# Kernel tuning notes

Measured on AMD Instinct MI355X. Metric: run time of the kernel, lower is better.

## Reference

```python
import jax, jax.numpy as jnp
import numpy as np

DILATION = 1  # module init dilation


def _pd_indexing1d(x, d, dilation):
    # x: (B, C, T) float; d: (B, 1, T) float pitch-dependent dilation factors
    B, C, T = x.shape
    dil = jnp.clip((d * dilation).astype(jnp.int32), 1)          # (B,1,T), min 1
    idx = jnp.arange(T, dtype=jnp.int32)[None, None, :]          # (1,1,T)
    idxP = jnp.abs(idx - dil) % T                                # past indices
    idxF0 = idx + dil
    # torch sets overflowed idx to -(idx % T) - 1, i.e. wraps to T - 1 - (idx % T)
    idxF = jnp.where(idxF0 >= T, T - 1 - (idxF0 % T), idxF0)     # future indices
    xP = jnp.take_along_axis(x, jnp.broadcast_to(idxP, x.shape), axis=2)
    xF = jnp.take_along_axis(x, jnp.broadcast_to(idxF, x.shape), axis=2)
    return xP, x, xF


def setup_inputs() -> dict:
    key = jax.random.key(0)
    k1, k2, k3, k4, k5, k6 = jax.random.split(key, 6)
    B, Cin, Cout, T = 8, 512, 512, 8192
    x = jax.random.normal(k1, (B, Cin, T), dtype=jnp.float32)
    d = jax.random.uniform(k2, (B, 1, T), dtype=jnp.float32)
    s = 1.0 / np.sqrt(Cin)
    W0 = jax.random.uniform(k3, (Cout, Cin), jnp.float32, -s, s)  # conv with bias
    b0 = jax.random.uniform(k4, (Cout,), jnp.float32, -s, s)
    W1 = jax.random.uniform(k5, (Cout, Cin), jnp.float32, -s, s)  # no bias
    W2 = jax.random.uniform(k6, (Cout, Cin), jnp.float32, -s, s)  # no bias
    return {"x": x, "d": d, "W0": W0, "b0": b0, "W1": W1, "W2": W2}


def reference(x, d, W0, b0, W1, W2):
    xP, xC, xF = _pd_indexing1d(x, d, DILATION)
    # three 1x1 convs (channel-mixing matmuls), summed; bias only on first conv
    out = jnp.einsum('oc,bct->bot', W0, xP) + b0[None, :, None]
    out = out + jnp.einsum('oc,bct->bot', W1, xC)
    out = out + jnp.einsum('oc,bct->bot', W2, xF)
    return out
```

## Files before the change

kernel.cpp:

```cpp
#include <hip/hip_runtime.h>

#define TT 8192
#define CIN 512
#define COUT 512
#define NB 8
#define KTOT 1536
#define NT 24

typedef __attribute__((ext_vector_type(4))) float f32x4;
typedef __attribute__((ext_vector_type(8))) short bf16x8;
typedef __attribute__((ext_vector_type(8))) unsigned short u16x8;

#define GLD16(g, l) __builtin_amdgcn_global_load_lds(                      \
    (const __attribute__((address_space(1))) void*)(g),                    \
    (__attribute__((address_space(3))) void*)(l), 16, 0, 0)

#define CFENCE() asm volatile("" ::: "memory")
#define SBAR() do { CFENCE(); __builtin_amdgcn_s_barrier(); CFENCE(); } while (0)
#define VMCNT4() asm volatile("s_waitcnt vmcnt(4)" ::: "memory")
#define VMCNT0() asm volatile("s_waitcnt vmcnt(0)" ::: "memory")
#define MFMA(a_, b_, c_) __builtin_amdgcn_mfma_f32_16x16x32_bf16((a_), (b_), (c_), 0, 0, 0)

__device__ inline unsigned short f2bf(float f) {
  union { float f; unsigned int u; } v; v.f = f;
  unsigned int u = v.u;
  unsigned int r = (u + 0x7FFFu + ((u >> 16) & 1u)) >> 16;
  return (unsigned short)r;
}

__global__ void k_convert_w(const float* __restrict__ W0, const float* __restrict__ W1,
                            const float* __restrict__ W2, unsigned short* __restrict__ Wb) {
  int i = blockIdx.x * 256 + threadIdx.x;
  if (i >= COUT * CIN) return;
  const float* Ws = blockIdx.y == 0 ? W0 : (blockIdx.y == 1 ? W1 : W2);
  int o = i >> 9, c = i & 511;
  Wb[(size_t)o * KTOT + blockIdx.y * CIN + c] = f2bf(Ws[i]);
}

__global__ void k_transpose(const float* __restrict__ x, unsigned short* __restrict__ xbT,
                            int b_base) {
  int b = b_base + blockIdx.z;
  const float* xb = x + (size_t)b * CIN * TT;
  unsigned short* xo = xbT + (size_t)blockIdx.z * TT * CIN;
  __shared__ float tile[64][65];
  int t0 = blockIdx.x * 64, c0 = blockIdx.y * 64;
  int tid = threadIdx.x;
#pragma unroll
  for (int it = 0; it < 16; ++it) {
    int L = it * 256 + tid;
    int c = L >> 6, t = L & 63;
    tile[c][t] = xb[(size_t)(c0 + c) * TT + (t0 + t)];
  }
  __syncthreads();
#pragma unroll
  for (int it = 0; it < 16; ++it) {
    int L = it * 256 + tid;
    int t = L >> 6, c = L & 63;
    xo[(size_t)(t0 + t) * CIN + (c0 + c)] = f2bf(tile[c][t]);
  }
}

__global__ __launch_bounds__(512) void k_gemm256(
    const unsigned short* __restrict__ Wb, const unsigned short* __restrict__ xbT,
    const float* __restrict__ d, const float* __restrict__ bias,
    float* __restrict__ out) {
  __shared__ __align__(16) unsigned short As[2][256 * 64];
  __shared__ __align__(16) unsigned short Bs[2][256 * 64];
  const int b = blockIdx.x;
  const int t0 = (blockIdx.y >> 1) * 256;
  const int row0 = (blockIdx.y & 1) * 256;
  const unsigned short* xb = xbT + (size_t)b * TT * CIN;
  const int tid = threadIdx.x;
  const int lane = tid & 63, wid = tid >> 6;
  const int wr = wid >> 2, wc = wid & 3;
  const int l15 = lane & 15, kg = lane >> 4;

  const int srow = tid >> 3;
  const int cSrc8 = (((tid & 7) ^ ((tid >> 4) & 7))) * 8;
  int aOff[4];
  int bOff[3][4];
#pragma unroll
  for (int j = 0; j < 4; ++j) {
    int r = j * 64 + srow;
    aOff[j] = (row0 + r) * KTOT + cSrc8;
    int t = t0 + r;
    float dv = d[(size_t)b * TT + t];
    int dil = (int)dv; if (dil < 1) dil = 1;
    int p = t - dil; if (p < 0) p = -p; p &= (TT - 1);
    int f0 = t + dil;
    int f = (f0 >= TT) ? (TT - 1 - (f0 & (TT - 1))) : f0;
    bOff[0][j] = p * CIN + cSrc8;
    bOff[1][j] = t * CIN + cSrc8;
    bOff[2][j] = f * CIN + cSrc8;
  }

  const int s7 = l15 >> 1;
  const int chunk0 = (kg ^ (s7 & 3)) + (s7 & 4);
  const int dK = (l15 & 8) ? -32 : 32;
  int aRd[2][4], bRd[2][2];
#pragma unroll
  for (int mh = 0; mh < 2; ++mh)
#pragma unroll
    for (int mi = 0; mi < 4; ++mi)
      aRd[mh][mi] = (wr * 128 + mh * 64 + mi * 16 + l15) * 64 + chunk0 * 8;
#pragma unroll
  for (int nh = 0; nh < 2; ++nh)
#pragma unroll
    for (int ni = 0; ni < 2; ++ni)
      bRd[nh][ni] = (wc * 64 + nh * 32 + ni * 16 + l15) * 64 + chunk0 * 8;

#define STAGE_A2(tc_, buf_, jp_) do {                                         \
    _Pragma("unroll") for (int j = 2 * (jp_); j < 2 * (jp_) + 2; ++j)         \
      GLD16(Wb + aOff[j] + (tc_) * 64, &As[buf_][j * 4096 + wid * 512]);      \
  } while (0)
#define STAGE_B2(tc_, buf_, jp_) do {                                         \
    _Pragma("unroll") for (int j = 2 * (jp_); j < 2 * (jp_) + 2; ++j)         \
      GLD16(xb + bOff[(tc_) >> 3][j] + ((tc_) & 7) * 64,                      \
            &Bs[buf_][j * 4096 + wid * 512]);                                 \
  } while (0)

  STAGE_A2(0, 0, 0); STAGE_A2(0, 0, 1);
  STAGE_B2(0, 0, 0); STAGE_B2(0, 0, 1);
  STAGE_B2(1, 1, 0); STAGE_B2(1, 1, 1);
  VMCNT4();
  SBAR();

  bf16x8 af0[4][2], af1[4][2], bfr[2][2];
  f32x4 acc[8][4] = {};

#pragma unroll 2
  for (int tc = 0; tc < NT; ++tc) {
    const int cur = tc & 1;
#pragma unroll
    for (int mi = 0; mi < 4; ++mi) {
      af0[mi][0] = *(const bf16x8*)&As[cur][aRd[0][mi]];
      af0[mi][1] = *(const bf16x8*)&As[cur][aRd[0][mi] + dK];
    }
#pragma unroll
    for (int ni = 0; ni < 2; ++ni) {
      bfr[ni][0] = *(const bf16x8*)&Bs[cur][bRd[0][ni]];
      bfr[ni][1] = *(const bf16x8*)&Bs[cur][bRd[0][ni] + dK];
    }
    if (tc + 1 < NT) STAGE_A2(tc + 1, cur ^ 1, 0);
    SBAR();
    __builtin_amdgcn_s_setprio(1);
#pragma unroll
    for (int mi = 0; mi < 4; ++mi)
#pragma unroll
      for (int ni = 0; ni < 2; ++ni) {
        acc[mi][ni] = MFMA(af0[mi][0], bfr[ni][0], acc[mi][ni]);
        acc[mi][ni] = MFMA(af0[mi][1], bfr[ni][1], acc[mi][ni]);
      }
    __builtin_amdgcn_s_setprio(0);
    SBAR();
#pragma unroll
    for (int mi = 0; mi < 4; ++mi) {
      af1[mi][0] = *(const bf16x8*)&As[cur][aRd[1][mi]];
      af1[mi][1] = *(const bf16x8*)&As[cur][aRd[1][mi] + dK];
    }
    if (tc + 1 < NT) STAGE_A2(tc + 1, cur ^ 1, 1);
    SBAR();
    __builtin_amdgcn_s_setprio(1);
#pragma unroll
    for (int mi = 0; mi < 4; ++mi)
#pragma unroll
      for (int ni = 0; ni < 2; ++ni) {
        acc[4 + mi][ni] = MFMA(af1[mi][0], bfr[ni][0], acc[4 + mi][ni]);
        acc[4 + mi][ni] = MFMA(af1[mi][1], bfr[ni][1], acc[4 + mi][ni]);
      }
    __builtin_amdgcn_s_setprio(0);
#pragma unroll
    for (int ni = 0; ni < 2; ++ni) {
      bfr[ni][0] = *(const bf16x8*)&Bs[cur][bRd[1][ni]];
      bfr[ni][1] = *(const bf16x8*)&Bs[cur][bRd[1][ni] + dK];
    }
    SBAR();
    __builtin_amdgcn_s_setprio(1);
#pragma unroll
    for (int mi = 0; mi < 4; ++mi)
#pragma unroll
      for (int ni = 0; ni < 2; ++ni) {
        acc[mi][2 + ni] = MFMA(af0[mi][0], bfr[ni][0], acc[mi][2 + ni]);
        acc[mi][2 + ni] = MFMA(af0[mi][1], bfr[ni][1], acc[mi][2 + ni]);
      }
    __builtin_amdgcn_s_setprio(0);
    if (tc + 2 < NT) { STAGE_B2(tc + 2, cur, 0); STAGE_B2(tc + 2, cur, 1); }
    __builtin_amdgcn_s_setprio(1);
#pragma unroll
    for (int mi = 0; mi < 4; ++mi)
#pragma unroll
      for (int ni = 0; ni < 2; ++ni) {
        acc[4 + mi][2 + ni] = MFMA(af1[mi][0], bfr[ni][0], acc[4 + mi][2 + ni]);
        acc[4 + mi][2 + ni] = MFMA(af1[mi][1], bfr[ni][1], acc[4 + mi][2 + ni]);
      }
    __builtin_amdgcn_s_setprio(0);
    if (tc + 2 < NT) { VMCNT4(); }
    else if (tc + 1 < NT) { VMCNT0(); }
    SBAR();
  }

  float* ob = out + (size_t)b * COUT * TT;
#pragma unroll
  for (int mh = 0; mh < 2; ++mh)
#pragma unroll
    for (int mi = 0; mi < 4; ++mi) {
      int m0 = row0 + wr * 128 + mh * 64 + mi * 16 + kg * 4;
#pragma unroll
      for (int nh = 0; nh < 2; ++nh)
#pragma unroll
        for (int ni = 0; ni < 2; ++ni) {
          int t = t0 + wc * 64 + nh * 32 + ni * 16 + l15;
          f32x4 v = acc[mh * 4 + mi][nh * 2 + ni];
#pragma unroll
          for (int j = 0; j < 4; ++j)
            ob[(size_t)(m0 + j) * TT + t] = v[j] + bias[m0 + j];
        }
    }
}

__global__ __launch_bounds__(256) void k_gemm(
    const unsigned short* __restrict__ Wb, const unsigned short* __restrict__ xbT,
    const float* __restrict__ d, const float* __restrict__ bias,
    float* __restrict__ out, int b_base) {
  __shared__ __align__(16) unsigned short As[128 * 32];
  __shared__ __align__(16) unsigned short Bs[128 * 32];
  int b = b_base + blockIdx.z;
  const unsigned short* xb = xbT + (size_t)blockIdx.z * TT * CIN;
  int row0 = blockIdx.x * 128;
  int t0 = blockIdx.y * 128;
  int tid = threadIdx.x;
  int lane = tid & 63, wid = tid >> 6;
  int wr = wid >> 1, wc = wid & 1;
  int l15 = lane & 15, kg = lane >> 4;
  int rs = tid >> 2, cch = tid & 3;

  const unsigned short* aw[2];
  const unsigned short* bw[2][3];
#pragma unroll
  for (int h = 0; h < 2; ++h) {
    int r = rs + h * 64;
    int cs = cch ^ ((r >> 1) & 3);
    aw[h] = Wb + (size_t)(row0 + r) * KTOT + cs * 8;
    int t = t0 + r;
    float dv = d[(size_t)b * TT + t];
    int dil = (int)dv; if (dil < 1) dil = 1;
    int p = t - dil; if (p < 0) p = -p; p &= (TT - 1);
    int f0 = t + dil;
    int f = (f0 >= TT) ? (TT - 1 - (f0 & (TT - 1))) : f0;
    bw[h][0] = xb + (size_t)p * CIN + cs * 8;
    bw[h][1] = xb + (size_t)t * CIN + cs * 8;
    bw[h][2] = xb + (size_t)f * CIN + cs * 8;
  }
  unsigned short* aDst[2];
  unsigned short* bDst[2];
#pragma unroll
  for (int h = 0; h < 2; ++h) {
    aDst[h] = As + h * 2048 + wid * 512;
    bDst[h] = Bs + h * 2048 + wid * 512;
  }
  int aoff[4], boff[4];
#pragma unroll
  for (int mi = 0; mi < 4; ++mi) {
    int r = wr * 64 + mi * 16 + l15;
    aoff[mi] = r * 32 + (kg ^ ((r >> 1) & 3)) * 8;
  }
#pragma unroll
  for (int ni = 0; ni < 4; ++ni) {
    int r = wc * 64 + ni * 16 + l15;
    boff[ni] = r * 32 + (kg ^ ((r >> 1) & 3)) * 8;
  }
  f32x4 acc[4][4] = {};
#pragma unroll
  for (int s = 0; s < 3; ++s) {
    for (int kt = 0; kt < 16; ++kt) {
      int koff = kt * 32;
#pragma unroll
      for (int h = 0; h < 2; ++h) {
        GLD16(aw[h] + s * CIN + koff, aDst[h]);
        GLD16(bw[h][s] + koff, bDst[h]);
      }
      __syncthreads();
      bf16x8 af[4], bf[4];
#pragma unroll
      for (int mi = 0; mi < 4; ++mi) af[mi] = *(const bf16x8*)(&As[aoff[mi]]);
#pragma unroll
      for (int ni = 0; ni < 4; ++ni) bf[ni] = *(const bf16x8*)(&Bs[boff[ni]]);
#pragma unroll
      for (int mi = 0; mi < 4; ++mi)
#pragma unroll
        for (int ni = 0; ni < 4; ++ni)
          acc[mi][ni] = MFMA(af[mi], bf[ni], acc[mi][ni]);
      __syncthreads();
    }
  }
  float* ob = out + (size_t)b * COUT * TT;
#pragma unroll
  for (int mi = 0; mi < 4; ++mi) {
    int m0 = row0 + wr * 64 + mi * 16 + kg * 4;
#pragma unroll
    for (int ni = 0; ni < 4; ++ni) {
      int t = t0 + wc * 64 + ni * 16 + l15;
#pragma unroll
      for (int j = 0; j < 4; ++j) {
        ob[(size_t)(m0 + j) * TT + t] = acc[mi][ni][j] + bias[m0 + j];
      }
    }
  }
}

extern "C" void kernel_launch(void* const* d_in, const int* in_sizes, int n_in,
                              void* d_out, int out_size, void* d_ws, size_t ws_size,
                              hipStream_t stream) {
  const float* x  = (const float*)d_in[0];
  const float* d  = (const float*)d_in[1];
  const float* W0 = (const float*)d_in[2];
  const float* b0 = (const float*)d_in[3];
  const float* W1 = (const float*)d_in[4];
  const float* W2 = (const float*)d_in[5];
  float* out = (float*)d_out;

  char* ws = (char*)d_ws;
  unsigned short* Wb  = (unsigned short*)ws;
  unsigned short* xbT = (unsigned short*)(ws + (2u << 20));
  const size_t SZ_XBT1 = (size_t)TT * CIN * 2;
  const size_t NEED_FULL = (size_t)(2u << 20) + (size_t)NB * SZ_XBT1;
  const size_t NEED_MIN  = (size_t)(2u << 20) + SZ_XBT1;

  if (ws_size >= NEED_MIN) {
    k_convert_w<<<dim3(1024, 3), 256, 0, stream>>>(W0, W1, W2, Wb);
    if (ws_size >= NEED_FULL) {
      k_transpose<<<dim3(TT / 64, CIN / 64, NB), 256, 0, stream>>>(x, xbT, 0);
      k_gemm256<<<dim3(NB, (TT / 256) * (COUT / 256), 1), 512, 0, stream>>>(
          Wb, xbT, d, b0, out);
    } else {
      for (int b = 0; b < NB; ++b) {
        k_transpose<<<dim3(TT / 64, CIN / 64, 1), 256, 0, stream>>>(x, xbT, b);
        k_gemm<<<dim3(COUT / 128, TT / 128, 1), 256, 0, stream>>>(Wb, xbT, d, b0, out, b);
      }
    }
  } else {
    for (int b = 0; b < NB; ++b) {
      k_transpose<<<dim3(TT / 64, CIN / 64, 1), 256, 0, stream>>>(x, xbT, b);
      k_gemm<<<dim3(COUT / 128, TT / 128, 1), 256, 0, stream>>>(Wb, xbT, d, b0, out, b);
    }
  }
}
```

Baseline: 144.8 us.

## Prefetch A tiles two stages ahead and cut barriers per K-step

Stages the weight (A) tiles two iterations ahead, like B, so both operands share the same double-buffer depth. The first fragment loads for the next iteration move to the end of the current iteration, which removes two of the four barriers in each K-step. An explicit lgkmcnt wait before the remaining barrier guards the LDS reads before that buffer is overwritten. The goal is to cut barrier stalls and overlap global-to-LDS copies with the MFMA work. In exchange more loads are in flight (vmcnt 8), and correctness depends on the hazard ordering of the LDS buffers.

```diff
diff --git a/kernel.cpp b/kernel.cpp
--- a/kernel.cpp
+++ b/kernel.cpp
@@ -17,8 +17,9 @@
 
 #define CFENCE() asm volatile("" ::: "memory")
 #define SBAR() do { CFENCE(); __builtin_amdgcn_s_barrier(); CFENCE(); } while (0)
-#define VMCNT4() asm volatile("s_waitcnt vmcnt(4)" ::: "memory")
+#define VMCNT8() asm volatile("s_waitcnt vmcnt(8)" ::: "memory")
 #define VMCNT0() asm volatile("s_waitcnt vmcnt(0)" ::: "memory")
+#define LGKM0() asm volatile("s_waitcnt lgkmcnt(0)" ::: "memory")
 #define MFMA(a_, b_, c_) __builtin_amdgcn_mfma_f32_16x16x32_bf16((a_), (b_), (c_), 0, 0, 0)
 
 __device__ inline unsigned short f2bf(float f) {
@@ -121,28 +122,33 @@
 
   STAGE_A2(0, 0, 0); STAGE_A2(0, 0, 1);
   STAGE_B2(0, 0, 0); STAGE_B2(0, 0, 1);
+  STAGE_A2(1, 1, 0); STAGE_A2(1, 1, 1);
   STAGE_B2(1, 1, 0); STAGE_B2(1, 1, 1);
-  VMCNT4();
+  VMCNT8();
   SBAR();
 
   bf16x8 af0[4][2], af1[4][2], bfr[2][2];
   f32x4 acc[8][4] = {};
+
+#pragma unroll
+  for (int mi = 0; mi < 4; ++mi) {
+    af0[mi][0] = *(const bf16x8*)&As[0][aRd[0][mi]];
+    af0[mi][1] = *(const bf16x8*)&As[0][aRd[0][mi] + dK];
+  }
+#pragma unroll
+  for (int ni = 0; ni < 2; ++ni) {
+    bfr[ni][0] = *(const bf16x8*)&Bs[0][bRd[0][ni]];
+    bfr[ni][1] = *(const bf16x8*)&Bs[0][bRd[0][ni] + dK];
+  }
 
 #pragma unroll 2
   for (int tc = 0; tc < NT; ++tc) {
     const int cur = tc & 1;
 #pragma unroll
     for (int mi = 0; mi < 4; ++mi) {
-      af0[mi][0] = *(const bf16x8*)&As[cur][aRd[0][mi]];
-      af0[mi][1] = *(const bf16x8*)&As[cur][aRd[0][mi] + dK];
-    }
-#pragma unroll
-    for (int ni = 0; ni < 2; ++ni) {
-      bfr[ni][0] = *(const bf16x8*)&Bs[cur][bRd[0][ni]];
-      bfr[ni][1] = *(const bf16x8*)&Bs[cur][bRd[0][ni] + dK];
-    }
-    if (tc + 1 < NT) STAGE_A2(tc + 1, cur ^ 1, 0);
-    SBAR();
+      af1[mi][0] = *(const bf16x8*)&As[cur][aRd[1][mi]];
+      af1[mi][1] = *(const bf16x8*)&As[cur][aRd[1][mi] + dK];
+    }
     __builtin_amdgcn_s_setprio(1);
 #pragma unroll
     for (int mi = 0; mi < 4; ++mi)
@@ -152,14 +158,6 @@
         acc[mi][ni] = MFMA(af0[mi][1], bfr[ni][1], acc[mi][ni]);
       }
     __builtin_amdgcn_s_setprio(0);
-    SBAR();
-#pragma unroll
-    for (int mi = 0; mi < 4; ++mi) {
-      af1[mi][0] = *(const bf16x8*)&As[cur][aRd[1][mi]];
-      af1[mi][1] = *(const bf16x8*)&As[cur][aRd[1][mi] + dK];
-    }
-    if (tc + 1 < NT) STAGE_A2(tc + 1, cur ^ 1, 1);
-    SBAR();
     __builtin_amdgcn_s_setprio(1);
 #pragma unroll
     for (int mi = 0; mi < 4; ++mi)
@@ -174,7 +172,9 @@
       bfr[ni][0] = *(const bf16x8*)&Bs[cur][bRd[1][ni]];
       bfr[ni][1] = *(const bf16x8*)&Bs[cur][bRd[1][ni] + dK];
     }
+    LGKM0();
     SBAR();
+    if (tc + 2 < NT) { STAGE_A2(tc + 2, cur, 0); STAGE_A2(tc + 2, cur, 1); }
     __builtin_amdgcn_s_setprio(1);
 #pragma unroll
     for (int mi = 0; mi < 4; ++mi)
@@ -194,9 +194,21 @@
         acc[4 + mi][2 + ni] = MFMA(af1[mi][1], bfr[ni][1], acc[4 + mi][2 + ni]);
       }
     __builtin_amdgcn_s_setprio(0);
-    if (tc + 2 < NT) { VMCNT4(); }
+    if (tc + 2 < NT) { VMCNT8(); }
     else if (tc + 1 < NT) { VMCNT0(); }
     SBAR();
+    if (tc + 1 < NT) {
+#pragma unroll
+      for (int mi = 0; mi < 4; ++mi) {
+        af0[mi][0] = *(const bf16x8*)&As[cur ^ 1][aRd[0][mi]];
+        af0[mi][1] = *(const bf16x8*)&As[cur ^ 1][aRd[0][mi] + dK];
+      }
+#pragma unroll
+      for (int ni = 0; ni < 2; ++ni) {
+        bfr[ni][0] = *(const bf16x8*)&Bs[cur ^ 1][bRd[0][ni]];
+        bfr[ni][1] = *(const bf16x8*)&Bs[cur ^ 1][bRd[0][ni] + dK];
+      }
+    }
   }
 
   float* ob = out + (size_t)b * COUT * TT;
```

Result: no change. 145.3 us (+0.3%).

## Load weight fragments directly from global into registers, drop A LDS staging

Applied to the files above, without the earlier changes.

Removes the LDS buffer for the weight (A) tile. Each wave now loads its MFMA A fragments straight from global memory into registers, one K-step ahead, and the vmcnt waits are retuned to the larger number of outstanding loads. This cuts LDS traffic, halves LDS usage and removes two barriers per iteration, which may allow more occupancy. In exchange, weight reads from global are duplicated across the waves sharing rows and now use uncoalesced 16-byte row-strided accesses, and the hand-set vmcnt counts must match the compiler's actual load ordering.

```diff
diff --git a/kernel.cpp b/kernel.cpp
--- a/kernel.cpp
+++ b/kernel.cpp
@@ -17,8 +17,10 @@
 
 #define CFENCE() asm volatile("" ::: "memory")
 #define SBAR() do { CFENCE(); __builtin_amdgcn_s_barrier(); CFENCE(); } while (0)
-#define VMCNT4() asm volatile("s_waitcnt vmcnt(4)" ::: "memory")
+#define VMCNT20() asm volatile("s_waitcnt vmcnt(20)" ::: "memory")
+#define VMCNT16() asm volatile("s_waitcnt vmcnt(16)" ::: "memory")
 #define VMCNT0() asm volatile("s_waitcnt vmcnt(0)" ::: "memory")
+#define LGKM0() asm volatile("s_waitcnt lgkmcnt(0)" ::: "memory")
 #define MFMA(a_, b_, c_) __builtin_amdgcn_mfma_f32_16x16x32_bf16((a_), (b_), (c_), 0, 0, 0)
 
 __device__ inline unsigned short f2bf(float f) {
@@ -64,7 +66,6 @@
     const unsigned short* __restrict__ Wb, const unsigned short* __restrict__ xbT,
     const float* __restrict__ d, const float* __restrict__ bias,
     float* __restrict__ out) {
-  __shared__ __align__(16) unsigned short As[2][256 * 64];
   __shared__ __align__(16) unsigned short Bs[2][256 * 64];
   const int b = blockIdx.x;
   const int t0 = (blockIdx.y >> 1) * 256;
@@ -77,13 +78,10 @@
 
   const int srow = tid >> 3;
   const int cSrc8 = (((tid & 7) ^ ((tid >> 4) & 7))) * 8;
-  int aOff[4];
   int bOff[3][4];
 #pragma unroll
   for (int j = 0; j < 4; ++j) {
-    int r = j * 64 + srow;
-    aOff[j] = (row0 + r) * KTOT + cSrc8;
-    int t = t0 + r;
+    int t = t0 + j * 64 + srow;
     float dv = d[(size_t)b * TT + t];
     int dil = (int)dv; if (dil < 1) dil = 1;
     int p = t - dil; if (p < 0) p = -p; p &= (TT - 1);
@@ -97,76 +95,65 @@
   const int s7 = l15 >> 1;
   const int chunk0 = (kg ^ (s7 & 3)) + (s7 & 4);
   const int dK = (l15 & 8) ? -32 : 32;
-  int aRd[2][4], bRd[2][2];
-#pragma unroll
-  for (int mh = 0; mh < 2; ++mh)
-#pragma unroll
-    for (int mi = 0; mi < 4; ++mi)
-      aRd[mh][mi] = (wr * 128 + mh * 64 + mi * 16 + l15) * 64 + chunk0 * 8;
+  int bRd[2][2];
 #pragma unroll
   for (int nh = 0; nh < 2; ++nh)
 #pragma unroll
     for (int ni = 0; ni < 2; ++ni)
       bRd[nh][ni] = (wc * 64 + nh * 32 + ni * 16 + l15) * 64 + chunk0 * 8;
 
-#define STAGE_A2(tc_, buf_, jp_) do {                                         \
-    _Pragma("unroll") for (int j = 2 * (jp_); j < 2 * (jp_) + 2; ++j)         \
-      GLD16(Wb + aOff[j] + (tc_) * 64, &As[buf_][j * 4096 + wid * 512]);      \
-  } while (0)
+  int aOffA[2][4];
+#pragma unroll
+  for (int mh = 0; mh < 2; ++mh)
+#pragma unroll
+    for (int mi = 0; mi < 4; ++mi)
+      aOffA[mh][mi] = (row0 + wr * 128 + mh * 64 + mi * 16 + l15) * KTOT + kg * 8;
+
 #define STAGE_B2(tc_, buf_, jp_) do {                                         \
     _Pragma("unroll") for (int j = 2 * (jp_); j < 2 * (jp_) + 2; ++j)         \
       GLD16(xb + bOff[(tc_) >> 3][j] + ((tc_) & 7) * 64,                      \
             &Bs[buf_][j * 4096 + wid * 512]);                                 \
   } while (0)
-
-  STAGE_A2(0, 0, 0); STAGE_A2(0, 0, 1);
+#define LOAD_A(mh_, tc_) do {                                                 \
+    _Pragma("unroll") for (int mi = 0; mi < 4; ++mi) {                        \
+      af[mh_][mi][0] = *(const bf16x8*)(Wb + aOffA[mh_][mi] + (tc_) * 64);    \
+      af[mh_][mi][1] = *(const bf16x8*)(Wb + aOffA[mh_][mi] + (tc_) * 64 + 32);\
+    }                                                                         \
+  } while (0)
+
+  bf16x8 af[2][4][2], bfr[2][2];
+  f32x4 acc[8][4] = {};
+
   STAGE_B2(0, 0, 0); STAGE_B2(0, 0, 1);
   STAGE_B2(1, 1, 0); STAGE_B2(1, 1, 1);
-  VMCNT4();
+  LOAD_A(0, 0); LOAD_A(1, 0);
+  VMCNT20();
   SBAR();
-
-  bf16x8 af0[4][2], af1[4][2], bfr[2][2];
-  f32x4 acc[8][4] = {};
 
 #pragma unroll 2
   for (int tc = 0; tc < NT; ++tc) {
     const int cur = tc & 1;
 #pragma unroll
-    for (int mi = 0; mi < 4; ++mi) {
-      af0[mi][0] = *(const bf16x8*)&As[cur][aRd[0][mi]];
-      af0[mi][1] = *(const bf16x8*)&As[cur][aRd[0][mi] + dK];
-    }
-#pragma unroll
     for (int ni = 0; ni < 2; ++ni) {
       bfr[ni][0] = *(const bf16x8*)&Bs[cur][bRd[0][ni]];
       bfr[ni][1] = *(const bf16x8*)&Bs[cur][bRd[0][ni] + dK];
     }
-    if (tc + 1 < NT) STAGE_A2(tc + 1, cur ^ 1, 0);
-    SBAR();
     __builtin_amdgcn_s_setprio(1);
 #pragma unroll
     for (int mi = 0; mi < 4; ++mi)
 #pragma unroll
       for (int ni = 0; ni < 2; ++ni) {
-        acc[mi][ni] = MFMA(af0[mi][0], bfr[ni][0], acc[mi][ni]);
-        acc[mi][ni] = MFMA(af0[mi][1], bfr[ni][1], acc[mi][ni]);
+        acc[mi][ni] = MFMA(af[0][mi][0], bfr[ni][0], acc[mi][ni]);
+        acc[mi][ni] = MFMA(af[0][mi][1], bfr[ni][1], acc[mi][ni]);
       }
     __builtin_amdgcn_s_setprio(0);
-    SBAR();
-#pragma unroll
-    for (int mi = 0; mi < 4; ++mi) {
-      af1[mi][0] = *(const bf16x8*)&As[cur][aRd[1][mi]];
-      af1[mi][1] = *(const bf16x8*)&As[cur][aRd[1][mi] + dK];
-    }
-    if (tc + 1 < NT) STAGE_A2(tc + 1, cur ^ 1, 1);
-    SBAR();
     __builtin_amdgcn_s_setprio(1);
 #pragma unroll
     for (int mi = 0; mi < 4; ++mi)
 #pragma unroll
       for (int ni = 0; ni < 2; ++ni) {
-        acc[4 + mi][ni] = MFMA(af1[mi][0], bfr[ni][0], acc[4 + mi][ni]);
-        acc[4 + mi][ni] = MFMA(af1[mi][1], bfr[ni][1], acc[4 + mi][ni]);
+        acc[4 + mi][ni] = MFMA(af[1][mi][0], bfr[ni][0], acc[4 + mi][ni]);
+        acc[4 + mi][ni] = MFMA(af[1][mi][1], bfr[ni][1], acc[4 + mi][ni]);
       }
     __builtin_amdgcn_s_setprio(0);
 #pragma unroll
@@ -174,28 +161,31 @@
       bfr[ni][0] = *(const bf16x8*)&Bs[cur][bRd[1][ni]];
       bfr[ni][1] = *(const bf16x8*)&Bs[cur][bRd[1][ni] + dK];
     }
+    __builtin_amdgcn_s_setprio(1);
+#pragma unroll
+    for (int mi = 0; mi < 4; ++mi)
+#pragma unroll
+      for (int ni = 0; ni < 2; ++ni) {
+        acc[mi][2 + ni] = MFMA(af[0][mi][0], bfr[ni][0], acc[mi][2 + ni]);
+        acc[mi][2 + ni] = MFMA(af[0][mi][1], bfr[ni][1], acc[mi][2 + ni]);
+      }
+    __builtin_amdgcn_s_setprio(0);
+    if (tc + 1 < NT) LOAD_A(0, tc + 1);
+    __builtin_amdgcn_s_setprio(1);
+#pragma unroll
+    for (int mi = 0; mi < 4; ++mi)
+#pragma unroll
+      for (int ni = 0; ni < 2; ++ni) {
+        acc[4 + mi][2 + ni] = MFMA(af[1][mi][0], bfr[ni][0], acc[4 + mi][2 + ni]);
+        acc[4 + mi][2 + ni] = MFMA(af[1][mi][1], bfr[ni][1], acc[4 + mi][2 + ni]);
+      }
+    __builtin_amdgcn_s_setprio(0);
+    if (tc + 1 < NT) LOAD_A(1, tc + 1);
+    LGKM0();
     SBAR();
-    __builtin_amdgcn_s_setprio(1);
-#pragma unroll
-    for (int mi = 0; mi < 4; ++mi)
-#pragma unroll
-      for (int ni = 0; ni < 2; ++ni) {
-        acc[mi][2 + ni] = MFMA(af0[mi][0], bfr[ni][0], acc[mi][2 + ni]);
-        acc[mi][2 + ni] = MFMA(af0[mi][1], bfr[ni][1], acc[mi][2 + ni]);
-      }
-    __builtin_amdgcn_s_setprio(0);
     if (tc + 2 < NT) { STAGE_B2(tc + 2, cur, 0); STAGE_B2(tc + 2, cur, 1); }
-    __builtin_amdgcn_s_setprio(1);
-#pragma unroll
-    for (int mi = 0; mi < 4; ++mi)
-#pragma unroll
-      for (int ni = 0; ni < 2; ++ni) {
-        acc[4 + mi][2 + ni] = MFMA(af1[mi][0], bfr[ni][0], acc[4 + mi][2 + ni]);
-        acc[4 + mi][2 + ni] = MFMA(af1[mi][1], bfr[ni][1], acc[4 + mi][2 + ni]);
-      }
-    __builtin_amdgcn_s_setprio(0);
-    if (tc + 2 < NT) { VMCNT4(); }
-    else if (tc + 1 < NT) { VMCNT0(); }
+    if (tc + 2 < NT) { VMCNT20(); }
+    else if (tc + 1 < NT) { VMCNT16(); }
     SBAR();
   }
 
```

Measured after the change: 271.2 us. 1.87x slower.
